# Kernel tuning notes

Hardware: AMD Instinct MI355X
Metric: run time of the kernel (lower is better)

The kernel has to match this reference:

```python
import jax, jax.numpy as jnp
import numpy as np

K = 4
HEADS = 4
IN_F = 128
OUT_F = 256
OUT_H = OUT_F // HEADS  # 64


def setup_inputs() -> dict:
    key = jax.random.key(0)
    ks = jax.random.split(key, 6)
    B, N = 8, 2048
    x = jax.random.normal(ks[0], (B, N, IN_F), dtype=jnp.float32)
    adj = jax.random.uniform(ks[1], (B, N, N), dtype=jnp.float32)
    # per-head linear: weight [H, out_h, in_f*(K+1)], bias [H, out_h]
    w_heads = 0.01 * jax.random.normal(ks[2], (HEADS, OUT_H, IN_F * (K + 1)), dtype=jnp.float32)
    b_heads = 0.01 * jax.random.normal(ks[3], (HEADS, OUT_H), dtype=jnp.float32)
    # final linear: [OUT_F, OUT_F]
    w_out = 0.01 * jax.random.normal(ks[4], (OUT_F, OUT_F), dtype=jnp.float32)
    b_out = 0.01 * jax.random.normal(ks[5], (OUT_F,), dtype=jnp.float32)
    return {"x": x, "adj": adj, "w_heads": w_heads, "b_heads": b_heads,
            "w_out": w_out, "b_out": b_out}


def _normalized_adj(adj):
    B, N, _ = adj.shape
    A_hat = adj + jnp.eye(N, dtype=adj.dtype)
    d = jnp.sum(A_hat, axis=2) ** -0.5          # [B, N]
    # L_hat = D^-1/2 A_hat D^-1/2 (diag scaling, no dense diag matmuls)
    return d[:, :, None] * A_hat * d[:, None, :]


def _legendre_stack(L, K):
    # elementwise Legendre recurrence on L; returns [B, N, N, K+1]
    P = [jnp.ones_like(L), L]
    for k in range(2, K + 1):
        P.append(((2 * k - 1) * L * P[-1] - (k - 1) * P[-2]) / k)
    return jnp.stack(P, axis=-1)


def reference(x, adj, w_heads, b_heads, w_out, b_out):
    B, N, F = x.shape
    L_hat = _normalized_adj(adj)                 # [B, N, N]
    LP = _legendre_stack(L_hat, K)               # [B, N, N, K+1] (shared by heads)
    # per-k propagation: cat([LP_k @ x for k], dim=2) -> k-major feature order
    prop = jnp.einsum('bnmk,bmf->bnkf', LP, x)   # [B, N, K+1, F]
    prop = prop.reshape(B, N, (K + 1) * F)       # [B, N, (K+1)*F]
    # per-head linear, concat heads along last dim (head-major)
    hout = jnp.einsum('bnc,hoc->bnho', prop, w_heads) + b_heads  # [B, N, H, out_h]
    hout = hout.reshape(B, N, HEADS * OUT_H)     # [B, N, OUT_F]
    return hout @ w_out.T + b_out                # [B, N, OUT_F]
```

## Files before the change

### kernel.cpp

```cpp
#include <hip/hip_runtime.h>
#include <hip/hip_bf16.h>
#include <stdint.h>

#define BATCH 8
#define NN    2048
#define FF    128
#define OUTF  256
#define C14   512

typedef unsigned short u16;
typedef u16  u16x8 __attribute__((ext_vector_type(8)));
typedef float f32x4 __attribute__((ext_vector_type(4)));

__device__ __forceinline__ u16 f2bf(float x) {
    union { float f; uint32_t u; } v; v.f = x;
    uint32_t r = v.u + 0x7FFFu + ((v.u >> 16) & 1u);
    return (u16)(r >> 16);
}
__device__ __forceinline__ uint32_t pack2(float a, float b) {
    return (uint32_t)f2bf(a) | ((uint32_t)f2bf(b) << 16);
}

__device__ __forceinline__ f32x4 mfma_bf16(u16x8 a, u16x8 b, f32x4 c) {
    asm("v_mfma_f32_16x16x32_bf16 %0, %1, %2, %0" : "+v"(c) : "v"(a), "v"(b));
    return c;
}

__global__ __launch_bounds__(256) void k_rowsum(const float* __restrict__ adj,
                                                float* __restrict__ dv) {
    size_t row = blockIdx.x;
    const float4* p = (const float4*)(adj + row * NN);
    int t = threadIdx.x;
    float4 v0 = p[t], v1 = p[t + 256];
    float s = v0.x + v0.y + v0.z + v0.w + v1.x + v1.y + v1.z + v1.w;
    #pragma unroll
    for (int off = 32; off > 0; off >>= 1) s += __shfl_down(s, off);
    __shared__ float r4[4];
    if ((t & 63) == 0) r4[t >> 6] = s;
    __syncthreads();
    if (t == 0) dv[row] = rsqrtf(r4[0] + r4[1] + r4[2] + r4[3] + 1.0f);
}

__global__ __launch_bounds__(256) void k_xprep(const float* __restrict__ x,
                                               u16* __restrict__ xT) {
    __shared__ u16 tile[FF][66];
    int b = blockIdx.x >> 5, mt = blockIdx.x & 31;
    const float* xb = x + ((size_t)(b * NN) + mt * 64) * FF;
    int t = threadIdx.x;
    #pragma unroll
    for (int i = 0; i < 32; ++i) {
        int idx = i * 256 + t;
        int ml = idx >> 7, f = idx & 127;
        tile[f][ml] = f2bf(xb[idx]);
    }
    __syncthreads();
    u16* xb2 = xT + (size_t)b * FF * NN + mt * 64;
    #pragma unroll
    for (int i = 0; i < 16; ++i) {
        int p = i * 256 + t;
        int f = p >> 5, mp = p & 31;
        uint32_t v = (uint32_t)tile[f][2 * mp] | ((uint32_t)tile[f][2 * mp + 1] << 16);
        *(uint32_t*)(xb2 + (size_t)f * NN + 2 * mp) = v;
    }
}

__global__ __launch_bounds__(256) void k_xpart(const float* __restrict__ x,
                                               float* __restrict__ part) {
    int b = blockIdx.x >> 4, j = blockIdx.x & 15;
    int t = threadIdx.x, f = t & 127, half = t >> 7;
    const float* xb = x + ((size_t)b * NN + j * 128 + half * 64) * FF;
    float s = 0.f;
    for (int m = 0; m < 64; ++m) s += xb[m * FF + f];
    __shared__ float red[256];
    red[t] = s; __syncthreads();
    if (t < 128) part[(size_t)blockIdx.x * FF + t] = red[t] + red[t + 128];
}

__global__ __launch_bounds__(256) void k_weff(const float* __restrict__ wh,
                                              const float* __restrict__ wo,
                                              float* __restrict__ weff0,
                                              u16* __restrict__ w14) {
    int o = blockIdx.x, t = threadIdx.x;
    __shared__ float wrow[256];
    wrow[t] = wo[o * 256 + t];
    __syncthreads();
    int c2 = (t < 128) ? (t + 512) : 639;
    float s0 = 0.f, s1 = 0.f, s2 = 0.f;
    for (int i = 0; i < 256; ++i) {
        float w = wrow[i];
        const float* row = wh + (size_t)i * 640;
        s0 = fmaf(w, row[t], s0);
        s1 = fmaf(w, row[t + 256], s1);
        s2 = fmaf(w, row[c2], s2);
    }
    if (t < 128) weff0[o * 128 + t] = s0;
    else         w14[(size_t)o * C14 + (t - 128)] = f2bf(s0);
    w14[(size_t)o * C14 + (t + 128)] = f2bf(s1);
    if (t < 128) w14[(size_t)o * C14 + (t + 384)] = f2bf(s2);
}

__global__ __launch_bounds__(256) void k_cb(const float* __restrict__ part,
                                            const float* __restrict__ weff0,
                                            const float* __restrict__ wo,
                                            const float* __restrict__ bh,
                                            const float* __restrict__ bo,
                                            float* __restrict__ cb) {
    int b = blockIdx.x, t = threadIdx.x;
    __shared__ float cs[128];
    __shared__ float bhl[256];
    if (t < 128) {
        float s = 0.f;
        for (int j = 0; j < 16; ++j) s += part[(size_t)(b * 16 + j) * FF + t];
        cs[t] = s;
    }
    bhl[t] = bh[t];
    __syncthreads();
    float s = bo[t];
    for (int i = 0; i < 256; ++i) s = fmaf(wo[(size_t)t * 256 + i], bhl[i], s);
    for (int f = 0; f < 128; ++f) s = fmaf(weff0[t * 128 + f], cs[f], s);
    cb[b * 256 + t] = s;
}

__global__ __launch_bounds__(256, 2) void k_main(const float* __restrict__ adj,
                                                 const float* __restrict__ dvec,
                                                 const u16* __restrict__ xT,
                                                 u16* __restrict__ prop) {
    __shared__ __align__(16) u16 Abuf[4 * 32 * 64];
    __shared__ __align__(16) u16 Bbuf[FF * 64];
    __shared__ float dn_l[32];

    int tid = threadIdx.x, lane = tid & 63, wv = tid >> 6;
    int bb = blockIdx.x >> 6, rt = blockIdx.x & 63;
    const float* adjb = adj + (size_t)bb * NN * NN + (size_t)(rt * 32) * NN;
    const u16* xTb = xT + (size_t)bb * FF * NN;
    if (tid < 32) dn_l[tid] = dvec[bb * NN + rt * 32 + tid];
    __syncthreads();

    int mp = tid & 31;
    f32x4 acc[2][8];
    #pragma unroll
    for (int mi = 0; mi < 2; ++mi)
        #pragma unroll
        for (int ni = 0; ni < 8; ++ni) acc[mi][ni] = (f32x4){0.f, 0.f, 0.f, 0.f};

    for (int ks = 0; ks < NN / 64; ++ks) {
        int mbase = ks * 64;
        #pragma unroll
        for (int it = 0; it < 4; ++it) {
            int ci = it * 256 + tid;
            int f = ci >> 3, c = ci & 7;
            u16x8 v = *(const u16x8*)(xTb + (size_t)f * NN + mbase + c * 8);
            *(u16x8*)((char*)Bbuf + f * 128 + ((c ^ (f & 7)) << 4)) = v;
        }
        float2 dmv = *(const float2*)(dvec + bb * NN + mbase + 2 * mp);
        #pragma unroll
        for (int i = 0; i < 4; ++i) {
            int r = i * 8 + (tid >> 5);
            int ng = rt * 32 + r;
            float2 av = *(const float2*)(adjb + (size_t)r * NN + mbase + 2 * mp);
            float dnv = dn_l[r];
            float a0 = av.x + ((mbase + 2 * mp)     == ng ? 1.f : 0.f);
            float a1 = av.y + ((mbase + 2 * mp + 1) == ng ? 1.f : 0.f);
            float L0 = a0 * dnv * dmv.x, L1 = a1 * dnv * dmv.y;
            float p2a = fmaf(1.5f * L0, L0, -0.5f);
            float p2b = fmaf(1.5f * L1, L1, -0.5f);
            float p3a = L0 * fmaf(1.66666667f, p2a, -0.66666667f);
            float p3b = L1 * fmaf(1.66666667f, p2b, -0.66666667f);
            float p4a = fmaf(1.75f * L0, p3a, -0.75f * p2a);
            float p4b = fmaf(1.75f * L1, p3b, -0.75f * p2b);
            uint32_t byteoff = (uint32_t)(r * 128 + (((mp * 4) ^ ((r & 7) << 4))));
            char* base = (char*)Abuf + byteoff;
            *(uint32_t*)(base)          = pack2(L0, L1);
            *(uint32_t*)(base + 4096)   = pack2(p2a, p2b);
            *(uint32_t*)(base + 8192)   = pack2(p3a, p3b);
            *(uint32_t*)(base + 12288)  = pack2(p4a, p4b);
        }
        __syncthreads();
        const char* Ab = (const char*)Abuf + (wv << 12);
        const char* Bb = (const char*)Bbuf;
        #pragma unroll
        for (int kk = 0; kk < 2; ++kk) {
            int ch = (kk << 2) + (lane >> 4);
            u16x8 af[2];
            #pragma unroll
            for (int mi = 0; mi < 2; ++mi) {
                int row = mi * 16 + (lane & 15);
                af[mi] = *(const u16x8*)(Ab + row * 128 + ((ch ^ (row & 7)) << 4));
            }
            #pragma unroll
            for (int ni = 0; ni < 8; ++ni) {
                int fr = ni * 16 + (lane & 15);
                u16x8 bf = *(const u16x8*)(Bb + fr * 128 + ((ch ^ (fr & 7)) << 4));
                acc[0][ni] = mfma_bf16(af[0], bf, acc[0][ni]);
                acc[1][ni] = mfma_bf16(af[1], bf, acc[1][ni]);
            }
        }
        __syncthreads();
    }
    asm volatile("s_nop 15\n\ts_nop 15");
    u16* pb = prop + ((size_t)bb * NN + rt * 32) * C14 + wv * 128;
    #pragma unroll
    for (int mi = 0; mi < 2; ++mi)
        #pragma unroll
        for (int ni = 0; ni < 8; ++ni) {
            int col = ni * 16 + (lane & 15);
            #pragma unroll
            for (int r4 = 0; r4 < 4; ++r4) {
                int row = mi * 16 + ((lane >> 4) << 2) + r4;
                pb[(size_t)row * C14 + col] = f2bf(acc[mi][ni][r4]);
            }
        }
}

__global__ __launch_bounds__(256, 2) void k_final(const u16* __restrict__ prop,
                                                  const u16* __restrict__ w14,
                                                  const float* __restrict__ cb,
                                                  float* __restrict__ out) {
    __shared__ __align__(16) u16 Abuf[32 * 64];
    __shared__ __align__(16) u16 Bbuf[256 * 64];
    int tid = threadIdx.x, lane = tid & 63, wv = tid >> 6;
    int rt = blockIdx.x, bb = rt >> 6;
    const u16* Ap = prop + (size_t)rt * 32 * C14;

    f32x4 acc[2][4];
    #pragma unroll
    for (int mi = 0; mi < 2; ++mi)
        #pragma unroll
        for (int ni = 0; ni < 4; ++ni) acc[mi][ni] = (f32x4){0.f, 0.f, 0.f, 0.f};

    for (int ks = 0; ks < 8; ++ks) {
        {
            int r = tid >> 3, c = tid & 7;
            u16x8 v = *(const u16x8*)(Ap + (size_t)r * C14 + ks * 64 + c * 8);
            *(u16x8*)((char*)Abuf + r * 128 + ((c ^ (r & 7)) << 4)) = v;
        }
        #pragma unroll
        for (int it = 0; it < 8; ++it) {
            int ci = it * 256 + tid;
            int o = ci >> 3, c = ci & 7;
            u16x8 v = *(const u16x8*)(w14 + (size_t)o * C14 + ks * 64 + c * 8);
            *(u16x8*)((char*)Bbuf + o * 128 + ((c ^ (o & 7)) << 4)) = v;
        }
        __syncthreads();
        #pragma unroll
        for (int kk = 0; kk < 2; ++kk) {
            int ch = (kk << 2) + (lane >> 4);
            u16x8 af[2];
            #pragma unroll
            for (int mi = 0; mi < 2; ++mi) {
                int row = mi * 16 + (lane & 15);
                af[mi] = *(const u16x8*)((char*)Abuf + row * 128 + ((ch ^ (row & 7)) << 4));
            }
            #pragma unroll
            for (int ni = 0; ni < 4; ++ni) {
                int o = wv * 64 + ni * 16 + (lane & 15);
                u16x8 bf = *(const u16x8*)((char*)Bbuf + o * 128 + ((ch ^ (o & 7)) << 4));
                acc[0][ni] = mfma_bf16(af[0], bf, acc[0][ni]);
                acc[1][ni] = mfma_bf16(af[1], bf, acc[1][ni]);
            }
        }
        __syncthreads();
    }
    asm volatile("s_nop 15\n\ts_nop 15");
    float* ob = out + (size_t)rt * 32 * OUTF;
    const float* cbb = cb + bb * OUTF + wv * 64;
    #pragma unroll
    for (int mi = 0; mi < 2; ++mi)
        #pragma unroll
        for (int ni = 0; ni < 4; ++ni) {
            int col = ni * 16 + (lane & 15);
            float cv = cbb[col];
            #pragma unroll
            for (int r4 = 0; r4 < 4; ++r4) {
                int row = mi * 16 + ((lane >> 4) << 2) + r4;
                ob[(size_t)row * OUTF + wv * 64 + col] = acc[mi][ni][r4] + cv;
            }
        }
}

extern "C" void kernel_launch(void* const* d_in, const int* in_sizes, int n_in,
                              void* d_out, int out_size, void* d_ws, size_t ws_size,
                              hipStream_t stream) {
    const float* x   = (const float*)d_in[0];
    const float* adj = (const float*)d_in[1];
    const float* wh  = (const float*)d_in[2];
    const float* bh  = (const float*)d_in[3];
    const float* wo  = (const float*)d_in[4];
    const float* bo  = (const float*)d_in[5];

    char* p = (char*)d_ws;
    float* dvec  = (float*)p;  p += (size_t)BATCH * NN * 4;
    u16*   xT    = (u16*)p;    p += (size_t)BATCH * FF * NN * 2;
    float* part  = (float*)p;  p += (size_t)128 * FF * 4;
    float* weff0 = (float*)p;  p += (size_t)OUTF * FF * 4;
    u16*   w14   = (u16*)p;    p += (size_t)OUTF * C14 * 2;
    float* cbv   = (float*)p;  p += (size_t)BATCH * OUTF * 4;
    u16*   prop  = (u16*)p;    p += (size_t)BATCH * NN * C14 * 2;

    k_rowsum<<<dim3(BATCH * NN), dim3(256), 0, stream>>>(adj, dvec);
    k_xprep <<<dim3(256),        dim3(256), 0, stream>>>(x, xT);
    k_xpart <<<dim3(128),        dim3(256), 0, stream>>>(x, part);
    k_weff  <<<dim3(256),        dim3(256), 0, stream>>>(wh, wo, weff0, w14);
    k_cb    <<<dim3(BATCH),      dim3(256), 0, stream>>>(part, weff0, wo, bh, bo, cbv);
    k_main  <<<dim3(512),        dim3(256), 0, stream>>>(adj, dvec, xT, prop);
    k_final <<<dim3(512),        dim3(256), 0, stream>>>(prop, w14, cbv, (float*)d_out);
}
```

Before: 314.8 us.

## Double-buffer main and final GEMM loops with register prefetch; fuse x column sums

Restructures k_main and k_final into a two-stage software pipeline. The next k-tile's global loads are held in registers while MFMAs consume the current LDS buffer, with LDS doubled to two buffers. The column-sum kernel is folded into the x transpose/convert kernel to drop a launch. bf16 packing now uses the hardware packed conversion intrinsic. The costs are higher LDS and register pressure, which may reduce occupancy or cause spills.

```diff
diff --git a/kernel.cpp b/kernel.cpp
--- a/kernel.cpp
+++ b/kernel.cpp
@@ -17,8 +17,9 @@
     uint32_t r = v.u + 0x7FFFu + ((v.u >> 16) & 1u);
     return (u16)(r >> 16);
 }
-__device__ __forceinline__ uint32_t pack2(float a, float b) {
-    return (uint32_t)f2bf(a) | ((uint32_t)f2bf(b) << 16);
+__device__ __forceinline__ uint32_t pk2(float a, float b) {
+    __hip_bfloat162 h = __float22bfloat162_rn(make_float2(a, b));
+    union { __hip_bfloat162 h; uint32_t u; } cv; cv.h = h; return cv.u;
 }
 
 __device__ __forceinline__ f32x4 mfma_bf16(u16x8 a, u16x8 b, f32x4 c) {
@@ -42,17 +43,23 @@
 }
 
 __global__ __launch_bounds__(256) void k_xprep(const float* __restrict__ x,
-                                               u16* __restrict__ xT) {
+                                               u16* __restrict__ xT,
+                                               float* __restrict__ part) {
     __shared__ u16 tile[FF][66];
+    __shared__ float red[256];
     int b = blockIdx.x >> 5, mt = blockIdx.x & 31;
     const float* xb = x + ((size_t)(b * NN) + mt * 64) * FF;
     int t = threadIdx.x;
+    float s = 0.f;
     #pragma unroll
     for (int i = 0; i < 32; ++i) {
         int idx = i * 256 + t;
         int ml = idx >> 7, f = idx & 127;
-        tile[f][ml] = f2bf(xb[idx]);
-    }
+        float v = xb[idx];
+        tile[f][ml] = f2bf(v);
+        s += v;
+    }
+    red[t] = s;
     __syncthreads();
     u16* xb2 = xT + (size_t)b * FF * NN + mt * 64;
     #pragma unroll
@@ -62,17 +69,6 @@
         uint32_t v = (uint32_t)tile[f][2 * mp] | ((uint32_t)tile[f][2 * mp + 1] << 16);
         *(uint32_t*)(xb2 + (size_t)f * NN + 2 * mp) = v;
     }
-}
-
-__global__ __launch_bounds__(256) void k_xpart(const float* __restrict__ x,
-                                               float* __restrict__ part) {
-    int b = blockIdx.x >> 4, j = blockIdx.x & 15;
-    int t = threadIdx.x, f = t & 127, half = t >> 7;
-    const float* xb = x + ((size_t)b * NN + j * 128 + half * 64) * FF;
-    float s = 0.f;
-    for (int m = 0; m < 64; ++m) s += xb[m * FF + f];
-    __shared__ float red[256];
-    red[t] = s; __syncthreads();
     if (t < 128) part[(size_t)blockIdx.x * FF + t] = red[t] + red[t + 128];
 }
 
@@ -110,7 +106,7 @@
     __shared__ float bhl[256];
     if (t < 128) {
         float s = 0.f;
-        for (int j = 0; j < 16; ++j) s += part[(size_t)(b * 16 + j) * FF + t];
+        for (int j = 0; j < 32; ++j) s += part[(size_t)(b * 32 + j) * FF + t];
         cs[t] = s;
     }
     bhl[t] = bh[t];
@@ -121,80 +117,110 @@
     cb[b * 256 + t] = s;
 }
 
+struct MRegs { u16x8 bv[4]; f32x4 av[2]; f32x4 dmv; };
+
+__device__ __forceinline__ void m_prefetch(MRegs& R, const u16* xTb, const float* adjb,
+                                           const float* dvb, int mbase, int tid) {
+    #pragma unroll
+    for (int it = 0; it < 4; ++it) {
+        int ci = it * 256 + tid; int f = ci >> 3, c = ci & 7;
+        R.bv[it] = *(const u16x8*)(xTb + (size_t)f * NN + mbase + c * 8);
+    }
+    int q = tid & 15;
+    R.dmv = *(const f32x4*)(dvb + mbase + q * 4);
+    #pragma unroll
+    for (int i = 0; i < 2; ++i) {
+        int r = i * 16 + (tid >> 4);
+        R.av[i] = *(const f32x4*)(adjb + (size_t)r * NN + mbase + q * 4);
+    }
+}
+
+__device__ __forceinline__ void m_commit(const MRegs& R, u16* Ab, u16* Bb,
+                                         const float* dn_l, int mbase, int rt, int tid) {
+    #pragma unroll
+    for (int it = 0; it < 4; ++it) {
+        int ci = it * 256 + tid; int f = ci >> 3, c = ci & 7;
+        *(u16x8*)((char*)Bb + f * 128 + ((c ^ (f & 7)) << 4)) = R.bv[it];
+    }
+    int q = tid & 15;
+    #pragma unroll
+    for (int i = 0; i < 2; ++i) {
+        int r = i * 16 + (tid >> 4);
+        int ng = rt * 32 + r - mbase - q * 4;
+        float dnv = dn_l[r];
+        float L[4], P2[4], P3[4], P4[4];
+        #pragma unroll
+        for (int j = 0; j < 4; ++j) {
+            float a = R.av[i][j] + ((j == ng) ? 1.f : 0.f);
+            L[j]  = a * dnv * R.dmv[j];
+            P2[j] = fmaf(1.5f * L[j], L[j], -0.5f);
+            P3[j] = L[j] * fmaf(1.66666667f, P2[j], -0.66666667f);
+            P4[j] = fmaf(1.75f * L[j], P3[j], -0.75f * P2[j]);
+        }
+        char* base = (char*)Ab + (uint32_t)(r * 128 + ((q * 8) ^ ((r & 7) << 4)));
+        *(uint2*)(base)         = make_uint2(pk2(L[0],  L[1]),  pk2(L[2],  L[3]));
+        *(uint2*)(base + 4096)  = make_uint2(pk2(P2[0], P2[1]), pk2(P2[2], P2[3]));
+        *(uint2*)(base + 8192)  = make_uint2(pk2(P3[0], P3[1]), pk2(P3[2], P3[3]));
+        *(uint2*)(base + 12288) = make_uint2(pk2(P4[0], P4[1]), pk2(P4[2], P4[3]));
+    }
+}
+
+__device__ __forceinline__ void m_mfma(const u16* A, const u16* B, int lane, f32x4 acc[2][8]) {
+    #pragma unroll
+    for (int kk = 0; kk < 2; ++kk) {
+        int ch = (kk << 2) + (lane >> 4);
+        u16x8 af[2];
+        #pragma unroll
+        for (int mi = 0; mi < 2; ++mi) {
+            int row = mi * 16 + (lane & 15);
+            af[mi] = *(const u16x8*)((const char*)A + row * 128 + ((ch ^ (row & 7)) << 4));
+        }
+        #pragma unroll
+        for (int ni = 0; ni < 8; ++ni) {
+            int fr = ni * 16 + (lane & 15);
+            u16x8 bf = *(const u16x8*)((const char*)B + fr * 128 + ((ch ^ (fr & 7)) << 4));
+            acc[0][ni] = mfma_bf16(af[0], bf, acc[0][ni]);
+            acc[1][ni] = mfma_bf16(af[1], bf, acc[1][ni]);
+        }
+    }
+}
+
 __global__ __launch_bounds__(256, 2) void k_main(const float* __restrict__ adj,
                                                  const float* __restrict__ dvec,
                                                  const u16* __restrict__ xT,
                                                  u16* __restrict__ prop) {
-    __shared__ __align__(16) u16 Abuf[4 * 32 * 64];
-    __shared__ __align__(16) u16 Bbuf[FF * 64];
+    __shared__ __align__(16) u16 Abuf[2][4 * 32 * 64];
+    __shared__ __align__(16) u16 Bbuf[2][FF * 64];
     __shared__ float dn_l[32];
 
     int tid = threadIdx.x, lane = tid & 63, wv = tid >> 6;
     int bb = blockIdx.x >> 6, rt = blockIdx.x & 63;
     const float* adjb = adj + (size_t)bb * NN * NN + (size_t)(rt * 32) * NN;
+    const float* dvb = dvec + bb * NN;
     const u16* xTb = xT + (size_t)bb * FF * NN;
+
+    f32x4 acc[2][8];
+    #pragma unroll
+    for (int mi = 0; mi < 2; ++mi)
+        #pragma unroll
+        for (int ni = 0; ni < 8; ++ni) acc[mi][ni] = (f32x4){0.f, 0.f, 0.f, 0.f};
+
+    MRegs R0, R1;
     if (tid < 32) dn_l[tid] = dvec[bb * NN + rt * 32 + tid];
-    __syncthreads();
-
-    int mp = tid & 31;
-    f32x4 acc[2][8];
-    #pragma unroll
-    for (int mi = 0; mi < 2; ++mi)
-        #pragma unroll
-        for (int ni = 0; ni < 8; ++ni) acc[mi][ni] = (f32x4){0.f, 0.f, 0.f, 0.f};
-
-    for (int ks = 0; ks < NN / 64; ++ks) {
-        int mbase = ks * 64;
-        #pragma unroll
-        for (int it = 0; it < 4; ++it) {
-            int ci = it * 256 + tid;
-            int f = ci >> 3, c = ci & 7;
-            u16x8 v = *(const u16x8*)(xTb + (size_t)f * NN + mbase + c * 8);
-            *(u16x8*)((char*)Bbuf + f * 128 + ((c ^ (f & 7)) << 4)) = v;
-        }
-        float2 dmv = *(const float2*)(dvec + bb * NN + mbase + 2 * mp);
-        #pragma unroll
-        for (int i = 0; i < 4; ++i) {
-            int r = i * 8 + (tid >> 5);
-            int ng = rt * 32 + r;
-            float2 av = *(const float2*)(adjb + (size_t)r * NN + mbase + 2 * mp);
-            float dnv = dn_l[r];
-            float a0 = av.x + ((mbase + 2 * mp)     == ng ? 1.f : 0.f);
-            float a1 = av.y + ((mbase + 2 * mp + 1) == ng ? 1.f : 0.f);
-            float L0 = a0 * dnv * dmv.x, L1 = a1 * dnv * dmv.y;
-            float p2a = fmaf(1.5f * L0, L0, -0.5f);
-            float p2b = fmaf(1.5f * L1, L1, -0.5f);
-            float p3a = L0 * fmaf(1.66666667f, p2a, -0.66666667f);
-            float p3b = L1 * fmaf(1.66666667f, p2b, -0.66666667f);
-            float p4a = fmaf(1.75f * L0, p3a, -0.75f * p2a);
-            float p4b = fmaf(1.75f * L1, p3b, -0.75f * p2b);
-            uint32_t byteoff = (uint32_t)(r * 128 + (((mp * 4) ^ ((r & 7) << 4))));
-            char* base = (char*)Abuf + byteoff;
-            *(uint32_t*)(base)          = pack2(L0, L1);
-            *(uint32_t*)(base + 4096)   = pack2(p2a, p2b);
-            *(uint32_t*)(base + 8192)   = pack2(p3a, p3b);
-            *(uint32_t*)(base + 12288)  = pack2(p4a, p4b);
-        }
+    m_prefetch(R0, xTb, adjb, dvb, 0, tid);
+    __syncthreads();
+    m_commit(R0, Abuf[0], Bbuf[0], dn_l, 0, rt, tid);
+    m_prefetch(R1, xTb, adjb, dvb, 64, tid);
+    __syncthreads();
+
+    for (int ks = 0; ks < 32; ks += 2) {
+        if (ks + 2 < 32) m_prefetch(R0, xTb, adjb, dvb, (ks + 2) * 64, tid);
+        m_commit(R1, Abuf[1], Bbuf[1], dn_l, (ks + 1) * 64, rt, tid);
+        m_mfma((const u16*)Abuf[0] + wv * 2048, (const u16*)Bbuf[0], lane, acc);
         __syncthreads();
-        const char* Ab = (const char*)Abuf + (wv << 12);
-        const char* Bb = (const char*)Bbuf;
-        #pragma unroll
-        for (int kk = 0; kk < 2; ++kk) {
-            int ch = (kk << 2) + (lane >> 4);
-            u16x8 af[2];
-            #pragma unroll
-            for (int mi = 0; mi < 2; ++mi) {
-                int row = mi * 16 + (lane & 15);
-                af[mi] = *(const u16x8*)(Ab + row * 128 + ((ch ^ (row & 7)) << 4));
-            }
-            #pragma unroll
-            for (int ni = 0; ni < 8; ++ni) {
-                int fr = ni * 16 + (lane & 15);
-                u16x8 bf = *(const u16x8*)(Bb + fr * 128 + ((ch ^ (fr & 7)) << 4));
-                acc[0][ni] = mfma_bf16(af[0], bf, acc[0][ni]);
-                acc[1][ni] = mfma_bf16(af[1], bf, acc[1][ni]);
-            }
-        }
+        if (ks + 3 < 32) m_prefetch(R1, xTb, adjb, dvb, (ks + 3) * 64, tid);
+        if (ks + 2 < 32) m_commit(R0, Abuf[0], Bbuf[0], dn_l, (ks + 2) * 64, rt, tid);
+        m_mfma((const u16*)Abuf[1] + wv * 2048, (const u16*)Bbuf[1], lane, acc);
         __syncthreads();
     }
     asm volatile("s_nop 15\n\ts_nop 15");
@@ -212,12 +238,54 @@
         }
 }
 
+struct FRegs { u16x8 a; u16x8 b[8]; };
+
+__device__ __forceinline__ void f_prefetch(FRegs& R, const u16* Ap, const u16* w14,
+                                           int mb, int tid) {
+    { int r = tid >> 3, c = tid & 7;
+      R.a = *(const u16x8*)(Ap + (size_t)r * C14 + mb + c * 8); }
+    #pragma unroll
+    for (int it = 0; it < 8; ++it) {
+        int ci = it * 256 + tid; int o = ci >> 3, c = ci & 7;
+        R.b[it] = *(const u16x8*)(w14 + (size_t)o * C14 + mb + c * 8);
+    }
+}
+__device__ __forceinline__ void f_commit(const FRegs& R, u16* FA, u16* FB, int tid) {
+    { int r = tid >> 3, c = tid & 7;
+      *(u16x8*)((char*)FA + r * 128 + ((c ^ (r & 7)) << 4)) = R.a; }
+    #pragma unroll
+    for (int it = 0; it < 8; ++it) {
+        int ci = it * 256 + tid; int o = ci >> 3, c = ci & 7;
+        *(u16x8*)((char*)FB + o * 128 + ((c ^ (o & 7)) << 4)) = R.b[it];
+    }
+}
+__device__ __forceinline__ void f_mfma(const u16* FA, const u16* FB, int lane, int wv,
+                                       f32x4 acc[2][4]) {
+    #pragma unroll
+    for (int kk = 0; kk < 2; ++kk) {
+        int ch = (kk << 2) + (lane >> 4);
+        u16x8 af[2];
+        #pragma unroll
+        for (int mi = 0; mi < 2; ++mi) {
+            int row = mi * 16 + (lane & 15);
+            af[mi] = *(const u16x8*)((const char*)FA + row * 128 + ((ch ^ (row & 7)) << 4));
+        }
+        #pragma unroll
+        for (int ni = 0; ni < 4; ++ni) {
+            int o = wv * 64 + ni * 16 + (lane & 15);
+            u16x8 bf = *(const u16x8*)((const char*)FB + o * 128 + ((ch ^ (o & 7)) << 4));
+            acc[0][ni] = mfma_bf16(af[0], bf, acc[0][ni]);
+            acc[1][ni] = mfma_bf16(af[1], bf, acc[1][ni]);
+        }
+    }
+}
+
 __global__ __launch_bounds__(256, 2) void k_final(const u16* __restrict__ prop,
                                                   const u16* __restrict__ w14,
                                                   const float* __restrict__ cb,
                                                   float* __restrict__ out) {
-    __shared__ __align__(16) u16 Abuf[32 * 64];
-    __shared__ __align__(16) u16 Bbuf[256 * 64];
+    __shared__ __align__(16) u16 FA[2][32 * 64];
+    __shared__ __align__(16) u16 FB[2][256 * 64];
     int tid = threadIdx.x, lane = tid & 63, wv = tid >> 6;
     int rt = blockIdx.x, bb = rt >> 6;
     const u16* Ap = prop + (size_t)rt * 32 * C14;
@@ -228,37 +296,20 @@
         #pragma unroll
         for (int ni = 0; ni < 4; ++ni) acc[mi][ni] = (f32x4){0.f, 0.f, 0.f, 0.f};
 
-    for (int ks = 0; ks < 8; ++ks) {
-        {
-            int r = tid >> 3, c = tid & 7;
-            u16x8 v = *(const u16x8*)(Ap + (size_t)r * C14 + ks * 64 + c * 8);
-            *(u16x8*)((char*)Abuf + r * 128 + ((c ^ (r & 7)) << 4)) = v;
-        }
-        #pragma unroll
-        for (int it = 0; it < 8; ++it) {
-            int ci = it * 256 + tid;
-            int o = ci >> 3, c = ci & 7;
-            u16x8 v = *(const u16x8*)(w14 + (size_t)o * C14 + ks * 64 + c * 8);
-            *(u16x8*)((char*)Bbuf + o * 128 + ((c ^ (o & 7)) << 4)) = v;
-        }
+    FRegs R0, R1;
+    f_prefetch(R0, Ap, w14, 0, tid);
+    f_commit(R0, FA[0], FB[0], tid);
+    f_prefetch(R1, Ap, w14, 64, tid);
+    __syncthreads();
+
+    for (int ks = 0; ks < 8; ks += 2) {
+        if (ks + 2 < 8) f_prefetch(R0, Ap, w14, (ks + 2) * 64, tid);
+        f_commit(R1, FA[1], FB[1], tid);
+        f_mfma(FA[0], FB[0], lane, wv, acc);
         __syncthreads();
-        #pragma unroll
-        for (int kk = 0; kk < 2; ++kk) {
-            int ch = (kk << 2) + (lane >> 4);
-            u16x8 af[2];
-            #pragma unroll
-            for (int mi = 0; mi < 2; ++mi) {
-                int row = mi * 16 + (lane & 15);
-                af[mi] = *(const u16x8*)((char*)Abuf + row * 128 + ((ch ^ (row & 7)) << 4));
-            }
-            #pragma unroll
-            for (int ni = 0; ni < 4; ++ni) {
-                int o = wv * 64 + ni * 16 + (lane & 15);
-                u16x8 bf = *(const u16x8*)((char*)Bbuf + o * 128 + ((ch ^ (o & 7)) << 4));
-                acc[0][ni] = mfma_bf16(af[0], bf, acc[0][ni]);
-                acc[1][ni] = mfma_bf16(af[1], bf, acc[1][ni]);
-            }
-        }
+        if (ks + 3 < 8) f_prefetch(R1, Ap, w14, (ks + 3) * 64, tid);
+        if (ks + 2 < 8) f_commit(R0, FA[0], FB[0], tid);
+        f_mfma(FA[1], FB[1], lane, wv, acc);
         __syncthreads();
     }
     asm volatile("s_nop 15\n\ts_nop 15");
@@ -291,15 +342,14 @@
     char* p = (char*)d_ws;
     float* dvec  = (float*)p;  p += (size_t)BATCH * NN * 4;
     u16*   xT    = (u16*)p;    p += (size_t)BATCH * FF * NN * 2;
-    float* part  = (float*)p;  p += (size_t)128 * FF * 4;
+    float* part  = (float*)p;  p += (size_t)256 * FF * 4;
     float* weff0 = (float*)p;  p += (size_t)OUTF * FF * 4;
     u16*   w14   = (u16*)p;    p += (size_t)OUTF * C14 * 2;
     float* cbv   = (float*)p;  p += (size_t)BATCH * OUTF * 4;
     u16*   prop  = (u16*)p;    p += (size_t)BATCH * NN * C14 * 2;
 
     k_rowsum<<<dim3(BATCH * NN), dim3(256), 0, stream>>>(adj, dvec);
-    k_xprep <<<dim3(256),        dim3(256), 0, stream>>>(x, xT);
-    k_xpart <<<dim3(128),        dim3(256), 0, stream>>>(x, part);
+    k_xprep <<<dim3(256),        dim3(256), 0, stream>>>(x, xT, part);
     k_weff  <<<dim3(256),        dim3(256), 0, stream>>>(wh, wo, weff0, w14);
     k_cb    <<<dim3(BATCH),      dim3(256), 0, stream>>>(part, weff0, wo, bh, bo, cbv);
     k_main  <<<dim3(512),        dim3(256), 0, stream>>>(adj, dvec, xT, prop);
```

Measured after the change: 304.8 us. 3.2% less time.
